# Optimization experiments

Measured on AMD Instinct MI355X. Metric: run time of the kernel, lower is better.

## Reference

```python
import jax, jax.numpy as jnp
import numpy as np

ENC_DIM = 128
DEC_DIM = 128
NUM_HEADS = 4
HEAD_DIM = DEC_DIM // NUM_HEADS


def _layernorm(x, g, b, eps=1e-5):
    mu = jnp.mean(x, axis=-1, keepdims=True)
    var = jnp.mean((x - mu) ** 2, axis=-1, keepdims=True)
    return (x - mu) * jax.lax.rsqrt(var + eps) * g + b


def setup_inputs() -> dict:
    key = jax.random.key(0)
    ks = jax.random.split(key, 12)
    B, H, W, D = 2, 16, 16, 16
    s = 0.02
    return {
        "encoder_feat": jax.random.normal(ks[0], (B, ENC_DIM, H, W, D), jnp.float32),
        "decoder_feat": jax.random.normal(ks[1], (B, DEC_DIM, H, W, D), jnp.float32),
        # torch Linear weights stored as [out, in]
        "Wq": jax.random.normal(ks[2], (DEC_DIM, DEC_DIM), jnp.float32) * s,
        "bq": jnp.zeros((DEC_DIM,), jnp.float32),
        "Wk": jax.random.normal(ks[3], (DEC_DIM, ENC_DIM), jnp.float32) * s,
        "bk": jnp.zeros((DEC_DIM,), jnp.float32),
        "Wv": jax.random.normal(ks[4], (DEC_DIM, ENC_DIM), jnp.float32) * s,
        "bv": jnp.zeros((DEC_DIM,), jnp.float32),
        "Wo": jax.random.normal(ks[5], (DEC_DIM, DEC_DIM), jnp.float32) * s,
        "bo": jnp.zeros((DEC_DIM,), jnp.float32),
        "g_enc": jnp.ones((ENC_DIM,), jnp.float32),
        "b_enc": jnp.zeros((ENC_DIM,), jnp.float32),
        "g_dec": jnp.ones((DEC_DIM,), jnp.float32),
        "b_dec": jnp.zeros((DEC_DIM,), jnp.float32),
        "g_out": jnp.ones((DEC_DIM,), jnp.float32),
        "b_out": jnp.zeros((DEC_DIM,), jnp.float32),
        "W1": jax.random.normal(ks[6], (DEC_DIM * 4, DEC_DIM), jnp.float32) * s,
        "b1": jnp.zeros((DEC_DIM * 4,), jnp.float32),
        "W2": jax.random.normal(ks[7], (DEC_DIM, DEC_DIM * 4), jnp.float32) * s,
        "b2": jnp.zeros((DEC_DIM,), jnp.float32),
    }


def reference(encoder_feat, decoder_feat, Wq, bq, Wk, bk, Wv, bv, Wo, bo,
              g_enc, b_enc, g_dec, b_dec, g_out, b_out, W1, b1, W2, b2):
    B, C_dec, H, W_, D = decoder_feat.shape
    N = H * W_ * D
    scale = HEAD_DIM ** -0.5
    # [B, C, H, W, D] -> [B, N, C]
    enc_seq = encoder_feat.reshape(B, -1, N).transpose(0, 2, 1)
    dec_seq = decoder_feat.reshape(B, C_dec, N).transpose(0, 2, 1)
    enc_seq = _layernorm(enc_seq, g_enc, b_enc)
    dec_seq = _layernorm(dec_seq, g_dec, b_dec)
    # projections (torch Linear: x @ W.T + b), split heads -> [B, h, N, d]
    Q = (dec_seq @ Wq.T + bq).reshape(B, N, NUM_HEADS, HEAD_DIM).transpose(0, 2, 1, 3)
    K = (enc_seq @ Wk.T + bk).reshape(B, N, NUM_HEADS, HEAD_DIM).transpose(0, 2, 1, 3)
    V = (enc_seq @ Wv.T + bv).reshape(B, N, NUM_HEADS, HEAD_DIM).transpose(0, 2, 1, 3)
    attn = jnp.einsum('bhqd,bhkd->bhqk', Q, K) * scale  # [B, h, N, N]
    attn = jax.nn.softmax(attn, axis=-1)
    out = jnp.einsum('bhqk,bhkd->bhqd', attn, V)
    out = out.transpose(0, 2, 1, 3).reshape(B, N, C_dec)
    out = out @ Wo.T + bo
    out = dec_seq + out
    h = _layernorm(out, g_out, b_out)
    ffn = jax.nn.gelu(h @ W1.T + b1, approximate=False) @ W2.T + b2
    out = out + ffn
    return out.transpose(0, 2, 1).reshape(B, C_dec, H, W_, D)
```

## Files before the change

kernel.cpp:

```cpp
#include <hip/hip_runtime.h>
#include <hip/hip_bf16.h>
#include <math.h>

#define B_ 2
#define N_ 4096
#define BN_ 8192
#define NH_ 4
#define SPLIT_ 8

using bf16x8   = __attribute__((ext_vector_type(8))) __bf16;
using f32x4    = __attribute__((ext_vector_type(4))) float;
using ushortx8 = __attribute__((ext_vector_type(8))) unsigned short;

#if __has_builtin(__builtin_amdgcn_exp2f)
#define FAST_EXP2(x) __builtin_amdgcn_exp2f(x)
#else
#define FAST_EXP2(x) __expf((x) * 0.6931471805599453f)
#endif

static __device__ __forceinline__ unsigned short f2bf(float f) {
    union { __hip_bfloat16 h; unsigned short u; } c;
    c.h = __float2bfloat16(f);
    return c.u;
}
static __device__ __forceinline__ float bf2f(unsigned short u) {
    union { __hip_bfloat16 h; unsigned short u; } c;
    c.u = u;
    return __bfloat162float(c.h);
}
static __device__ __forceinline__ unsigned int pk2bf(float lo, float hi) {
    return __builtin_amdgcn_perm(__float_as_uint(hi) + 0x8000u,
                                 __float_as_uint(lo) + 0x8000u, 0x07060302u);
}
static __device__ __forceinline__ bf16x8 ldw(const float* __restrict__ W, size_t off) {
    const float4 a = *(const float4*)(W + off);
    const float4 b = *(const float4*)(W + off + 4);
    union { uint4 u; bf16x8 v; } c;
    c.u.x = pk2bf(a.x, a.y); c.u.y = pk2bf(a.z, a.w);
    c.u.z = pk2bf(b.x, b.y); c.u.w = pk2bf(b.z, b.w);
    return c.v;
}

__global__ __launch_bounds__(256)
void qkv3_kernel(const float* __restrict__ enc, const float* __restrict__ dec,
                 const float* __restrict__ g_enc, const float* __restrict__ b_enc,
                 const float* __restrict__ g_dec, const float* __restrict__ b_dec,
                 const float* __restrict__ Wq, const float* __restrict__ Wk,
                 const float* __restrict__ Wv,
                 const float* __restrict__ bq, const float* __restrict__ bk,
                 const float* __restrict__ bv,
                 const float* __restrict__ Wo, const float* __restrict__ W1,
                 const float* __restrict__ W2,
                 unsigned short* __restrict__ wo, unsigned short* __restrict__ w1,
                 unsigned short* __restrict__ w2,
                 unsigned short* __restrict__ Qh, unsigned short* __restrict__ Kh,
                 unsigned short* __restrict__ Vt,
                 unsigned short* __restrict__ dec_lnb) {
    const int t = threadIdx.x;
    if (blockIdx.x >= 512) {
        const int e = ((int)blockIdx.x - 512) * 256 * 8 + t * 8;
        const float* src; unsigned short* dst; int off;
        if (e < 16384)       { src = Wo; dst = wo; off = e; }
        else if (e < 81920)  { src = W1; dst = w1; off = e - 16384; }
        else                 { src = W2; dst = w2; off = e - 81920; }
        const float4 a = *(const float4*)(src + off);
        const float4 b = *(const float4*)(src + off + 4);
        uint4 p;
        p.x = pk2bf(a.x, a.y); p.y = pk2bf(a.z, a.w);
        p.z = pk2bf(b.x, b.y); p.w = pk2bf(b.z, b.w);
        *(uint4*)(dst + off) = p;
        return;
    }
    __shared__ float tile[128][33];
    __shared__ float mu_s[32], inv_s[32];
    const int z  = blockIdx.x >> 8;
    const int m0 = (blockIdx.x & 255) * 32;
    const int b  = m0 >> 12, n0 = m0 & 4095;
    const float* inb   = ((z == 0) ? dec : enc) + (size_t)b * 128 * N_;
    const float* gamma = (z == 0) ? g_dec : g_enc;
    const float* beta  = (z == 0) ? b_dec : b_enc;

    {
        const int col = t & 31;
        const int r0  = t >> 5;
        #pragma unroll
        for (int j = 0; j < 16; ++j) {
            const int r = r0 + 8 * j;
            tile[r][col] = inb[(size_t)r * N_ + n0 + col];
        }
    }
    __syncthreads();
    {
        const int tok = t >> 3;
        const int ln  = t & 7;
        float s = 0.f, ss = 0.f;
        for (int c = ln; c < 128; c += 8) {
            const float x = tile[c][tok];
            s += x; ss += x * x;
        }
        for (int m = 1; m < 8; m <<= 1) {
            s  += __shfl_xor(s, m);
            ss += __shfl_xor(ss, m);
        }
        if (ln == 0) {
            const float mu  = s * (1.f / 128.f);
            mu_s[tok]  = mu;
            inv_s[tok] = rsqrtf(ss * (1.f / 128.f) - mu * mu + 1e-5f);
        }
    }
    __syncthreads();

    const int wvx = t >> 6, lane = t & 63;
    const int l15 = lane & 15, quad = lane >> 4;
    const int tokgrp  = (wvx & 1) * 16;
    const int colbase = (z == 0) ? (wvx >> 1) * 64 : 0;
    const bool isV    = (z == 1) && (wvx >> 1);
    const bool wrLN   = (z == 0) && ((wvx >> 1) == 0);
    const int nbCount = (z == 0) ? 4 : 8;
    const int tok = tokgrp + l15;
    const float mu  = mu_s[tok];
    const float inv = inv_s[tok];

    bf16x8 af[4];
    #pragma unroll
    for (int kk = 0; kk < 4; ++kk) {
        float y[8];
        #pragma unroll
        for (int j = 0; j < 8; ++j) {
            const int c = kk * 32 + quad * 8 + j;
            y[j] = (tile[c][tok] - mu) * inv * gamma[c] + beta[c];
        }
        union { uint4 u; bf16x8 v8; ushortx8 us; } cvt;
        cvt.u.x = pk2bf(y[0], y[1]); cvt.u.y = pk2bf(y[2], y[3]);
        cvt.u.z = pk2bf(y[4], y[5]); cvt.u.w = pk2bf(y[6], y[7]);
        af[kk] = cvt.v8;
        if (wrLN)
            *(ushortx8*)(dec_lnb + (size_t)(m0 + tok) * 128 + kk * 32 + quad * 8) = cvt.us;
    }

    const float* Wb   = (z == 0) ? Wq : (isV ? Wv : Wk);
    const float* bias = (z == 0) ? bq : (isV ? bv : bk);
    const float sc = (z == 0) ? (0.17677669529663687f * 1.4426950408889634f) : 1.f;
    const int nbase = n0 + tokgrp + quad * 4;

    #pragma unroll
    for (int nb = 0; nb < 8; ++nb) {
        if (nb >= nbCount) break;
        const int col = colbase + nb * 16 + l15;
        f32x4 a = {0.f, 0.f, 0.f, 0.f};
        #pragma unroll
        for (int kk = 0; kk < 4; ++kk) {
            const bf16x8 wf = ldw(Wb, (size_t)col * 128 + kk * 32 + quad * 8);
            a = __builtin_amdgcn_mfma_f32_16x16x32_bf16(af[kk], wf, a, 0, 0, 0);
        }
        const int h = col >> 5, d = col & 31;
        const float bz = bias[col];
        if (isV) {
            ushort4 pk;
            pk.x = f2bf(a[0] + bz);
            pk.y = f2bf(a[1] + bz);
            pk.z = f2bf(a[2] + bz);
            pk.w = f2bf(a[3] + bz);
            *(ushort4*)(Vt + ((size_t)(b * NH_ + h) * 32 + d) * N_ + nbase) = pk;
        } else {
            unsigned short* dst = (z == 0) ? Qh : Kh;
            #pragma unroll
            for (int r = 0; r < 4; ++r)
                dst[((size_t)(b * NH_ + h) * N_ + nbase + r) * 32 + d] = f2bf((a[r] + bz) * sc);
        }
    }
}

__global__ __launch_bounds__(512)
void attn_kernel7(const unsigned short* __restrict__ Qh,
                  const unsigned short* __restrict__ Kh,
                  const unsigned short* __restrict__ Vt,
                  unsigned short* __restrict__ ctx) {
    __shared__ alignas(16) unsigned short sP[8][64][72];
    __shared__ float ldsL[8][64];

    const int gid  = blockIdx.x;
    const int bh   = gid & 7;
    const int qblk = gid >> 3;
    const int t  = threadIdx.x;
    const int wvx = t >> 6, lane = t & 63;
    const int l15 = lane & 15, quad = lane >> 4;
    const int s = wvx;
    const int qw = qblk * 64;
    const size_t hbse = (size_t)bh * N_ * 32;

    bf16x8 qf[4];
    #pragma unroll
    for (int f = 0; f < 4; ++f)
        qf[f] = *(const bf16x8*)(Qh + hbse + (size_t)(qw + f * 16 + l15) * 32 + quad * 8);

    const unsigned short* Kp = Kh + hbse;
    const unsigned short* Vp = Vt + (size_t)bh * 32 * N_;

    f32x4 o0[4], o1[4];
    float l[4];
    #pragma unroll
    for (int f = 0; f < 4; ++f) {
        o0[f] = f32x4{0.f, 0.f, 0.f, 0.f};
        o1[f] = f32x4{0.f, 0.f, 0.f, 0.f};
        l[f] = 0.f;
    }
    const f32x4 zero = {0.f, 0.f, 0.f, 0.f};

    const int kbeg = s * (N_ / SPLIT_);
    const int kend = kbeg + (N_ / SPLIT_);

    bf16x8 kf[4];
    #pragma unroll
    for (int c = 0; c < 4; ++c)
        kf[c] = *(const bf16x8*)(Kp + (size_t)(kbeg + c * 16 + l15) * 32 + quad * 8);

    for (int k0 = kbeg; k0 < kend; k0 += 64) {
        bf16x8 va[2], vb[2];
        #pragma unroll
        for (int s2 = 0; s2 < 2; ++s2) {
            va[s2] = *(const bf16x8*)(Vp + (size_t)l15 * N_        + k0 + s2 * 32 + quad * 8);
            vb[s2] = *(const bf16x8*)(Vp + (size_t)(16 + l15) * N_ + k0 + s2 * 32 + quad * 8);
        }
        const int kn = (k0 + 64 < kend) ? (k0 + 64) : kbeg;
        bf16x8 kfn[4];
        #pragma unroll
        for (int c = 0; c < 4; ++c)
            kfn[c] = *(const bf16x8*)(Kp + (size_t)(kn + c * 16 + l15) * 32 + quad * 8);

        #pragma unroll
        for (int f = 0; f < 4; ++f) {
            #pragma unroll
            for (int c = 0; c < 4; ++c) {
                const f32x4 sv = __builtin_amdgcn_mfma_f32_16x16x32_bf16(kf[c], qf[f], zero, 0, 0, 0);
                const float p0 = FAST_EXP2(sv[0]);
                const float p1 = FAST_EXP2(sv[1]);
                const float p2 = FAST_EXP2(sv[2]);
                const float p3 = FAST_EXP2(sv[3]);
                l[f] += (p0 + p1) + (p2 + p3);
                uint2 pk;
                pk.x = pk2bf(p0, p1);
                pk.y = pk2bf(p2, p3);
                *(uint2*)&sP[wvx][f * 16 + l15][c * 16 + quad * 4] = pk;
            }
        }
        #pragma unroll
        for (int f = 0; f < 4; ++f) {
            #pragma unroll
            for (int s2 = 0; s2 < 2; ++s2) {
                const bf16x8 pf = *(const bf16x8*)&sP[wvx][f * 16 + l15][s2 * 32 + quad * 8];
                o0[f] = __builtin_amdgcn_mfma_f32_16x16x32_bf16(va[s2], pf, o0[f], 0, 0, 0);
                o1[f] = __builtin_amdgcn_mfma_f32_16x16x32_bf16(vb[s2], pf, o1[f], 0, 0, 0);
            }
        }
        #pragma unroll
        for (int c = 0; c < 4; ++c) kf[c] = kfn[c];
    }

    float lf4[4];
    #pragma unroll
    for (int f = 0; f < 4; ++f) {
        float lf = l[f];
        lf += __shfl_xor(lf, 16);
        lf += __shfl_xor(lf, 32);
        lf4[f] = lf;
    }

    __syncthreads();
    float* ldsO = (float*)&sP[0][0][0];
    #pragma unroll
    for (int f = 0; f < 4; ++f) {
        const int q = f * 16 + l15;
        float* row = ldsO + ((size_t)s * 64 + q) * 36;
        *(f32x4*)(row + quad * 4)      = o0[f];
        *(f32x4*)(row + 16 + quad * 4) = o1[f];
        if (quad == 0) ldsL[s][q] = lf4[f];
    }
    __syncthreads();

    const int tok = t >> 3;
    const int d0  = (t & 7) * 4;
    f32x4 sum = {0.f, 0.f, 0.f, 0.f};
    float lsum = 0.f;
    #pragma unroll
    for (int w = 0; w < 8; ++w) {
        sum  += *(const f32x4*)(ldsO + ((size_t)w * 64 + tok) * 36 + d0);
        lsum += ldsL[w][tok];
    }
    const float inv = 1.f / lsum;
    uint2 pk;
    pk.x = pk2bf(sum[0] * inv, sum[1] * inv);
    pk.y = pk2bf(sum[2] * inv, sum[3] * inv);
    const int b = bh >> 2, h = bh & 3;
    *(uint2*)(ctx + ((size_t)(b * N_ + qw + tok)) * 128 + h * 32 + d0) = pk;
}

__global__ __launch_bounds__(256)
void fused_tail4_kernel(const unsigned short* __restrict__ ctx,
                        const unsigned short* __restrict__ wo,
                        const float* __restrict__ bo,
                        const unsigned short* __restrict__ decb,
                        const float* __restrict__ g, const float* __restrict__ be,
                        const unsigned short* __restrict__ w1,
                        const float* __restrict__ b1,
                        const unsigned short* __restrict__ w2,
                        const float* __restrict__ b2,
                        float* __restrict__ out) {
    __shared__ alignas(16) unsigned short sredb[4][64][36];
    __shared__ float sln[4][2][16];
    __shared__ alignas(16) unsigned short hb_lds[16][136];
    __shared__ alignas(16) unsigned short smid[16][536];
    const int t = threadIdx.x;
    const int wv = t >> 6, lane = t & 63;
    const int l15 = lane & 15, quad = lane >> 4;
    const int m0 = blockIdx.x * 16;

    const int tokA = m0 + l15;
    const bf16x8 af = *(const bf16x8*)(ctx + (size_t)tokA * 128 + wv * 32 + quad * 8);

    #pragma unroll
    for (int nb = 0; nb < 8; ++nb) {
        const bf16x8 wf = *(const bf16x8*)(wo + (size_t)(nb * 16 + l15) * 128
                                           + wv * 32 + quad * 8);
        const f32x4 a = __builtin_amdgcn_mfma_f32_16x16x32_bf16(
            af, wf, f32x4{0.f, 0.f, 0.f, 0.f}, 0, 0, 0);
        uint2 p;
        p.x = pk2bf(a[0], a[1]);
        p.y = pk2bf(a[2], a[3]);
        *(uint2*)&sredb[wv][lane][nb * 4] = p;
    }
    __syncthreads();

    float v[2][4];
    #pragma unroll
    for (int lnb = 0; lnb < 2; ++lnb) {
        const int nbg = 2 * wv + lnb;
        f32x4 p = {0.f, 0.f, 0.f, 0.f};
        #pragma unroll
        for (int w = 0; w < 4; ++w) {
            const ushort4 u = *(const ushort4*)&sredb[w][lane][nbg * 4];
            p[0] += bf2f(u.x); p[1] += bf2f(u.y);
            p[2] += bf2f(u.z); p[3] += bf2f(u.w);
        }
        const int col = nbg * 16 + l15;
        const float bz = bo[col];
        #pragma unroll
        for (int r = 0; r < 4; ++r) {
            const int tok = m0 + quad * 4 + r;
            v[lnb][r] = p[r] + bz + bf2f(decb[(size_t)tok * 128 + col]);
        }
    }

    {
        float s[4], ss[4];
        #pragma unroll
        for (int r = 0; r < 4; ++r) {
            float a = v[0][r] + v[1][r];
            float b = v[0][r] * v[0][r] + v[1][r] * v[1][r];
            for (int m = 1; m < 16; m <<= 1) {
                a += __shfl_xor(a, m);
                b += __shfl_xor(b, m);
            }
            s[r] = a; ss[r] = b;
        }
        if (l15 == 0) {
            #pragma unroll
            for (int r = 0; r < 4; ++r) {
                sln[wv][0][quad * 4 + r] = s[r];
                sln[wv][1][quad * 4 + r] = ss[r];
            }
        }
    }
    __syncthreads();

    {
        #pragma unroll
        for (int r = 0; r < 4; ++r) {
            const int tk = quad * 4 + r;
            const float stot  = sln[0][0][tk] + sln[1][0][tk] + sln[2][0][tk] + sln[3][0][tk];
            const float sstot = sln[0][1][tk] + sln[1][1][tk] + sln[2][1][tk] + sln[3][1][tk];
            const float mu  = stot * (1.f / 128.f);
            const float inv = rsqrtf(sstot * (1.f / 128.f) - mu * mu + 1e-5f);
            #pragma unroll
            for (int lnb = 0; lnb < 2; ++lnb) {
                const int col = (2 * wv + lnb) * 16 + l15;
                hb_lds[tk][col] = f2bf((v[lnb][r] - mu) * inv * g[col] + be[col]);
            }
        }
    }
    __syncthreads();

    bf16x8 hf[4];
    #pragma unroll
    for (int kk = 0; kk < 4; ++kk)
        hf[kk] = *(const bf16x8*)&hb_lds[l15][kk * 32 + quad * 8];
    #pragma unroll
    for (int nb = 0; nb < 8; ++nb) {
        const int col = wv * 128 + nb * 16 + l15;
        f32x4 a = {0.f, 0.f, 0.f, 0.f};
        #pragma unroll
        for (int kk = 0; kk < 4; ++kk) {
            const bf16x8 wf = *(const bf16x8*)(w1 + (size_t)col * 128 + kk * 32 + quad * 8);
            a = __builtin_amdgcn_mfma_f32_16x16x32_bf16(hf[kk], wf, a, 0, 0, 0);
        }
        const float bz = b1[col];
        #pragma unroll
        for (int r = 0; r < 4; ++r) {
            float x = a[r] + bz;
            x = 0.5f * x * (1.f + erff(x * 0.70710678118f));
            smid[quad * 4 + r][col] = f2bf(x);
        }
    }
    __syncthreads();

    f32x4 acc[8];
    #pragma unroll
    for (int nb = 0; nb < 8; ++nb) acc[nb] = f32x4{0.f, 0.f, 0.f, 0.f};
    #pragma unroll
    for (int kk = 0; kk < 4; ++kk) {
        const bf16x8 af2 = *(const bf16x8*)&smid[l15][wv * 128 + kk * 32 + quad * 8];
        #pragma unroll
        for (int nb = 0; nb < 8; ++nb) {
            const bf16x8 wf = *(const bf16x8*)(w2 + (size_t)(nb * 16 + l15) * 512
                                               + wv * 128 + kk * 32 + quad * 8);
            acc[nb] = __builtin_amdgcn_mfma_f32_16x16x32_bf16(af2, wf, acc[nb], 0, 0, 0);
        }
    }
    __syncthreads();
    #pragma unroll
    for (int nb = 0; nb < 8; ++nb) {
        uint2 p;
        p.x = pk2bf(acc[nb][0], acc[nb][1]);
        p.y = pk2bf(acc[nb][2], acc[nb][3]);
        *(uint2*)&sredb[wv][lane][nb * 4] = p;
    }
    __syncthreads();

    {
        const int b = m0 >> 12;
        const int nb0 = (m0 & 4095) + quad * 4;
        #pragma unroll
        for (int lnb = 0; lnb < 2; ++lnb) {
            const int nbg = 2 * wv + lnb;
            f32x4 p = {0.f, 0.f, 0.f, 0.f};
            #pragma unroll
            for (int w = 0; w < 4; ++w) {
                const ushort4 u = *(const ushort4*)&sredb[w][lane][nbg * 4];
                p[0] += bf2f(u.x); p[1] += bf2f(u.y);
                p[2] += bf2f(u.z); p[3] += bf2f(u.w);
            }
            const int col = nbg * 16 + l15;
            const float bz = b2[col];
            f32x4 res;
            #pragma unroll
            for (int r = 0; r < 4; ++r)
                res[r] = p[r] + bz + v[lnb][r];
            *(f32x4*)&out[((size_t)(b * 128 + col)) * N_ + nb0] = res;
        }
    }
}

extern "C" void kernel_launch(void* const* d_in, const int* in_sizes, int n_in,
                              void* d_out, int out_size, void* d_ws, size_t ws_size,
                              hipStream_t stream) {
    const float* enc   = (const float*)d_in[0];
    const float* dec   = (const float*)d_in[1];
    const float* Wq    = (const float*)d_in[2];
    const float* bq    = (const float*)d_in[3];
    const float* Wk    = (const float*)d_in[4];
    const float* bk    = (const float*)d_in[5];
    const float* Wv    = (const float*)d_in[6];
    const float* bv    = (const float*)d_in[7];
    const float* Wo    = (const float*)d_in[8];
    const float* bo    = (const float*)d_in[9];
    const float* g_enc = (const float*)d_in[10];
    const float* b_enc = (const float*)d_in[11];
    const float* g_dec = (const float*)d_in[12];
    const float* b_dec = (const float*)d_in[13];
    const float* g_out = (const float*)d_in[14];
    const float* b_out = (const float*)d_in[15];
    const float* W1    = (const float*)d_in[16];
    const float* b1    = (const float*)d_in[17];
    const float* W2    = (const float*)d_in[18];
    const float* b2    = (const float*)d_in[19];
    float* out = (float*)d_out;
    char*  W   = (char*)d_ws;

    unsigned short* wob = (unsigned short*)(W);
    unsigned short* w1b = wob + 16384;
    unsigned short* w2b = w1b + 65536;
    unsigned short* dec_lnb = (unsigned short*)(W + (2560ull << 10));
    unsigned short* Qh      = (unsigned short*)(W + (4608ull << 10));
    unsigned short* Kh      = (unsigned short*)(W + (6656ull << 10));
    unsigned short* Vt      = (unsigned short*)(W + (8704ull << 10));
    unsigned short* ctx     = (unsigned short*)(W + (10752ull << 10));

    qkv3_kernel<<<512 + 72, 256, 0, stream>>>(
        enc, dec, g_enc, b_enc, g_dec, b_dec, Wq, Wk, Wv, bq, bk, bv,
        Wo, W1, W2, wob, w1b, w2b, Qh, Kh, Vt, dec_lnb);

    attn_kernel7<<<512, 512, 0, stream>>>(Qh, Kh, Vt, ctx);

    fused_tail4_kernel<<<512, 256, 0, stream>>>(ctx, wob, bo, dec_lnb,
                                                g_out, b_out, w1b, b1, w2b, b2, out);
}
```

Measured before the change: 166.0 us.

## Split QKV projection into three block groups; replace split-K reductions with full-K MFMA

The QKV kernel now launches 768 projection blocks, one group each for Q, K and V. Each wave handles four column tiles, where before the K/V blocks computed both K and V with eight tiles per wave. This spreads the per-block work more evenly, but the encoder tile load and its layernorm are now done twice, once for K and once for V. In the tail kernel, the Wo and W2 GEMMs drop the split-K scheme: each wave accumulates the full K dimension for its own output columns, removing the LDS reduction buffer, the bf16 rounding of partial sums and extra barriers, at the cost of more serial MFMA chains and more weight loads per wave.

```diff
diff --git a/kernel.cpp b/kernel.cpp
--- a/kernel.cpp
+++ b/kernel.cpp
@@ -42,7 +42,7 @@
 }
 
 __global__ __launch_bounds__(256)
-void qkv3_kernel(const float* __restrict__ enc, const float* __restrict__ dec,
+void qkv4_kernel(const float* __restrict__ enc, const float* __restrict__ dec,
                  const float* __restrict__ g_enc, const float* __restrict__ b_enc,
                  const float* __restrict__ g_dec, const float* __restrict__ b_dec,
                  const float* __restrict__ Wq, const float* __restrict__ Wk,
@@ -57,8 +57,8 @@
                  unsigned short* __restrict__ Vt,
                  unsigned short* __restrict__ dec_lnb) {
     const int t = threadIdx.x;
-    if (blockIdx.x >= 512) {
-        const int e = ((int)blockIdx.x - 512) * 256 * 8 + t * 8;
+    if (blockIdx.x >= 768) {
+        const int e = ((int)blockIdx.x - 768) * 2048 + t * 8;
         const float* src; unsigned short* dst; int off;
         if (e < 16384)       { src = Wo; dst = wo; off = e; }
         else if (e < 81920)  { src = W1; dst = w1; off = e - 16384; }
@@ -113,10 +113,8 @@
     const int wvx = t >> 6, lane = t & 63;
     const int l15 = lane & 15, quad = lane >> 4;
     const int tokgrp  = (wvx & 1) * 16;
-    const int colbase = (z == 0) ? (wvx >> 1) * 64 : 0;
-    const bool isV    = (z == 1) && (wvx >> 1);
+    const int colbase = (wvx >> 1) * 64;
     const bool wrLN   = (z == 0) && ((wvx >> 1) == 0);
-    const int nbCount = (z == 0) ? 4 : 8;
     const int tok = tokgrp + l15;
     const float mu  = mu_s[tok];
     const float inv = inv_s[tok];
@@ -138,14 +136,13 @@
             *(ushortx8*)(dec_lnb + (size_t)(m0 + tok) * 128 + kk * 32 + quad * 8) = cvt.us;
     }
 
-    const float* Wb   = (z == 0) ? Wq : (isV ? Wv : Wk);
-    const float* bias = (z == 0) ? bq : (isV ? bv : bk);
+    const float* Wb   = (z == 0) ? Wq : ((z == 1) ? Wk : Wv);
+    const float* bias = (z == 0) ? bq : ((z == 1) ? bk : bv);
     const float sc = (z == 0) ? (0.17677669529663687f * 1.4426950408889634f) : 1.f;
     const int nbase = n0 + tokgrp + quad * 4;
 
     #pragma unroll
-    for (int nb = 0; nb < 8; ++nb) {
-        if (nb >= nbCount) break;
+    for (int nb = 0; nb < 4; ++nb) {
         const int col = colbase + nb * 16 + l15;
         f32x4 a = {0.f, 0.f, 0.f, 0.f};
         #pragma unroll
@@ -155,7 +152,7 @@
         }
         const int h = col >> 5, d = col & 31;
         const float bz = bias[col];
-        if (isV) {
+        if (z == 2) {
             ushort4 pk;
             pk.x = f2bf(a[0] + bz);
             pk.y = f2bf(a[1] + bz);
@@ -296,7 +293,7 @@
 }
 
 __global__ __launch_bounds__(256)
-void fused_tail4_kernel(const unsigned short* __restrict__ ctx,
+void fused_tail5_kernel(const unsigned short* __restrict__ ctx,
                         const unsigned short* __restrict__ wo,
                         const float* __restrict__ bo,
                         const unsigned short* __restrict__ decb,
@@ -306,7 +303,6 @@
                         const unsigned short* __restrict__ w2,
                         const float* __restrict__ b2,
                         float* __restrict__ out) {
-    __shared__ alignas(16) unsigned short sredb[4][64][36];
     __shared__ float sln[4][2][16];
     __shared__ alignas(16) unsigned short hb_lds[16][136];
     __shared__ alignas(16) unsigned short smid[16][536];
@@ -316,38 +312,26 @@
     const int m0 = blockIdx.x * 16;
 
     const int tokA = m0 + l15;
-    const bf16x8 af = *(const bf16x8*)(ctx + (size_t)tokA * 128 + wv * 32 + quad * 8);
-
-    #pragma unroll
-    for (int nb = 0; nb < 8; ++nb) {
-        const bf16x8 wf = *(const bf16x8*)(wo + (size_t)(nb * 16 + l15) * 128
-                                           + wv * 32 + quad * 8);
-        const f32x4 a = __builtin_amdgcn_mfma_f32_16x16x32_bf16(
-            af, wf, f32x4{0.f, 0.f, 0.f, 0.f}, 0, 0, 0);
-        uint2 p;
-        p.x = pk2bf(a[0], a[1]);
-        p.y = pk2bf(a[2], a[3]);
-        *(uint2*)&sredb[wv][lane][nb * 4] = p;
-    }
-    __syncthreads();
+    bf16x8 af[4];
+    #pragma unroll
+    for (int kk = 0; kk < 4; ++kk)
+        af[kk] = *(const bf16x8*)(ctx + (size_t)tokA * 128 + kk * 32 + quad * 8);
 
     float v[2][4];
     #pragma unroll
     for (int lnb = 0; lnb < 2; ++lnb) {
-        const int nbg = 2 * wv + lnb;
-        f32x4 p = {0.f, 0.f, 0.f, 0.f};
-        #pragma unroll
-        for (int w = 0; w < 4; ++w) {
-            const ushort4 u = *(const ushort4*)&sredb[w][lane][nbg * 4];
-            p[0] += bf2f(u.x); p[1] += bf2f(u.y);
-            p[2] += bf2f(u.z); p[3] += bf2f(u.w);
-        }
-        const int col = nbg * 16 + l15;
+        const int col = (2 * wv + lnb) * 16 + l15;
+        f32x4 a = {0.f, 0.f, 0.f, 0.f};
+        #pragma unroll
+        for (int kk = 0; kk < 4; ++kk) {
+            const bf16x8 wf = *(const bf16x8*)(wo + (size_t)col * 128 + kk * 32 + quad * 8);
+            a = __builtin_amdgcn_mfma_f32_16x16x32_bf16(af[kk], wf, a, 0, 0, 0);
+        }
         const float bz = bo[col];
         #pragma unroll
         for (int r = 0; r < 4; ++r) {
             const int tok = m0 + quad * 4 + r;
-            v[lnb][r] = p[r] + bz + bf2f(decb[(size_t)tok * 128 + col]);
+            v[lnb][r] = a[r] + bz + bf2f(decb[(size_t)tok * 128 + col]);
         }
     }
 
@@ -413,50 +397,24 @@
     }
     __syncthreads();
 
-    f32x4 acc[8];
-    #pragma unroll
-    for (int nb = 0; nb < 8; ++nb) acc[nb] = f32x4{0.f, 0.f, 0.f, 0.f};
-    #pragma unroll
-    for (int kk = 0; kk < 4; ++kk) {
-        const bf16x8 af2 = *(const bf16x8*)&smid[l15][wv * 128 + kk * 32 + quad * 8];
-        #pragma unroll
-        for (int nb = 0; nb < 8; ++nb) {
-            const bf16x8 wf = *(const bf16x8*)(w2 + (size_t)(nb * 16 + l15) * 512
-                                               + wv * 128 + kk * 32 + quad * 8);
-            acc[nb] = __builtin_amdgcn_mfma_f32_16x16x32_bf16(af2, wf, acc[nb], 0, 0, 0);
-        }
-    }
-    __syncthreads();
-    #pragma unroll
-    for (int nb = 0; nb < 8; ++nb) {
-        uint2 p;
-        p.x = pk2bf(acc[nb][0], acc[nb][1]);
-        p.y = pk2bf(acc[nb][2], acc[nb][3]);
-        *(uint2*)&sredb[wv][lane][nb * 4] = p;
-    }
-    __syncthreads();
-
-    {
-        const int b = m0 >> 12;
-        const int nb0 = (m0 & 4095) + quad * 4;
-        #pragma unroll
-        for (int lnb = 0; lnb < 2; ++lnb) {
-            const int nbg = 2 * wv + lnb;
-            f32x4 p = {0.f, 0.f, 0.f, 0.f};
-            #pragma unroll
-            for (int w = 0; w < 4; ++w) {
-                const ushort4 u = *(const ushort4*)&sredb[w][lane][nbg * 4];
-                p[0] += bf2f(u.x); p[1] += bf2f(u.y);
-                p[2] += bf2f(u.z); p[3] += bf2f(u.w);
-            }
-            const int col = nbg * 16 + l15;
-            const float bz = b2[col];
-            f32x4 res;
-            #pragma unroll
-            for (int r = 0; r < 4; ++r)
-                res[r] = p[r] + bz + v[lnb][r];
-            *(f32x4*)&out[((size_t)(b * 128 + col)) * N_ + nb0] = res;
-        }
+    const int b = m0 >> 12;
+    const int nb0 = (m0 & 4095) + quad * 4;
+    #pragma unroll
+    for (int lnb = 0; lnb < 2; ++lnb) {
+        const int col = (2 * wv + lnb) * 16 + l15;
+        f32x4 a = {0.f, 0.f, 0.f, 0.f};
+        #pragma unroll
+        for (int kk = 0; kk < 16; ++kk) {
+            const bf16x8 af2 = *(const bf16x8*)&smid[l15][kk * 32 + quad * 8];
+            const bf16x8 wf  = *(const bf16x8*)(w2 + (size_t)col * 512 + kk * 32 + quad * 8);
+            a = __builtin_amdgcn_mfma_f32_16x16x32_bf16(af2, wf, a, 0, 0, 0);
+        }
+        const float bz = b2[col];
+        f32x4 res;
+        #pragma unroll
+        for (int r = 0; r < 4; ++r)
+            res[r] = a[r] + bz + v[lnb][r];
+        *(f32x4*)&out[((size_t)(b * 128 + col)) * N_ + nb0] = res;
     }
 }
 
@@ -495,12 +453,12 @@
     unsigned short* Vt      = (unsigned short*)(W + (8704ull << 10));
     unsigned short* ctx     = (unsigned short*)(W + (10752ull << 10));
 
-    qkv3_kernel<<<512 + 72, 256, 0, stream>>>(
+    qkv4_kernel<<<768 + 72, 256, 0, stream>>>(
         enc, dec, g_enc, b_enc, g_dec, b_dec, Wq, Wk, Wv, bq, bk, bv,
         Wo, W1, W2, wob, w1b, w2b, Qh, Kh, Vt, dec_lnb);
 
     attn_kernel7<<<512, 512, 0, stream>>>(Qh, Kh, Vt, ctx);
 
-    fused_tail4_kernel<<<512, 256, 0, stream>>>(ctx, wob, bo, dec_lnb,
+    fused_tail5_kernel<<<512, 256, 0, stream>>>(ctx, wob, bo, dec_lnb,
                                                 g_out, b_out, w1b, b1, w2b, b2, out);
 }
```

Result: no change. 168.0 us (+1.3%).
